# Optimization experiments

Measured on AMD Instinct MI355X. Metric: run time of the kernel, lower is better.

## Reference

```python
import jax, jax.numpy as jnp
import numpy as np

N = 4096          # num_nodes
F = 64            # node_features
H = 128           # hidden_dim
NH = 4            # num_heads
HD = H // NH      # per-head dim = 32
L = 3             # num_layers
C = 7             # num_classes
EDGE_P = 0.004    # ~16 avg degree


def setup_inputs() -> dict:
    key = jax.random.key(0)
    ks = jax.random.split(key, 20)
    g = lambda k, shape, fan_in: jax.random.normal(k, shape, jnp.float32) / np.sqrt(fan_in)
    x = jax.random.normal(ks[0], (N, F), jnp.float32)
    adj = (jax.random.uniform(ks[1], (N, N)) < EDGE_P).astype(jnp.float32)
    return {
        "x": x,
        "adj": adj,
        "enc_W": g(ks[2], (F, H), F), "enc_b": jnp.zeros((H,), jnp.float32),
        "gcn_W": g(ks[3], (L, H, H), H), "gcn_b": jnp.zeros((L, H), jnp.float32),
        "attn_W": g(ks[4], (L, NH, H, HD), H), "attn_Wb": jnp.zeros((L, NH, HD), jnp.float32),
        "attn_a": g(ks[5], (L, NH, 2 * HD), 2 * HD), "attn_ab": jnp.zeros((L, NH), jnp.float32),
        "cls_W1": g(ks[6], (H, H // 2), H), "cls_b1": jnp.zeros((H // 2,), jnp.float32),
        "cls_W2": g(ks[7], (H // 2, C), H // 2), "cls_b2": jnp.zeros((C,), jnp.float32),
        "con_W1": g(ks[8], (H, H // 2), H), "con_b1": jnp.zeros((H // 2,), jnp.float32),
        "con_W2": g(ks[9], (H // 2, 1), H // 2), "con_b2": jnp.zeros((1,), jnp.float32),
    }


def _normalize_adj(adj):
    a = adj + jnp.eye(adj.shape[0], dtype=adj.dtype)
    dinv = jnp.sum(a, axis=1) ** -0.5
    return dinv[:, None] * a * dinv[None, :]


def _gcn(h, adj_norm, W, b):
    support = adj_norm @ h                      # [N,H]
    return jax.nn.relu(support @ W + b)         # dropout=0 (eval)


def _attention(h, edge_mask, W, Wb, a, ab):
    # h:[N,H], W:[NH,H,HD], a:[NH,2*HD]; per-pair score = Linear(concat(h_i,h_j))
    hh = jnp.einsum('nf,hfd->hnd', h, W) + Wb[:, None, :]     # [NH,N,HD]
    a_src, a_dst = a[:, :HD], a[:, HD:]
    s_src = jnp.einsum('hnd,hd->hn', hh, a_src)               # [NH,N]
    s_dst = jnp.einsum('hnd,hd->hn', hh, a_dst)               # [NH,N]
    scores = s_src[:, :, None] + s_dst[:, None, :] + ab[:, None, None]
    # original uses literal 0.0 (NOT -inf) for non-edges before softmax
    scores = jnp.where(edge_mask[None, :, :], scores, 0.0)    # [NH,N,N]
    probs = jax.nn.softmax(scores, axis=-1)
    out = jnp.einsum('hij,hjd->hid', probs, hh)               # [NH,N,HD]
    return out.transpose(1, 0, 2).reshape(h.shape[0], NH * HD)


def reference(x, adj, enc_W, enc_b, gcn_W, gcn_b, attn_W, attn_Wb, attn_a, attn_ab,
              cls_W1, cls_b1, cls_W2, cls_b2, con_W1, con_b1, con_W2, con_b2):
    h = jax.nn.relu(x @ enc_W + enc_b)          # node encoder (dropout=0)
    adj_norm = _normalize_adj(adj)
    edge_mask = adj > 0
    for i in range(L):
        h_gcn = _gcn(h, adj_norm, gcn_W[i], gcn_b[i])
        h_attn = _attention(h, edge_mask, attn_W[i], attn_Wb[i], attn_a[i], attn_ab[i])
        h = jax.nn.relu(h_gcn + h_attn)
    node_logits = jax.nn.relu(h @ cls_W1 + cls_b1) @ cls_W2 + cls_b2
    h_mean = jnp.mean(h, axis=0, keepdims=True)
    contagion = jax.nn.relu(h_mean @ con_W1 + con_b1) @ con_W2 + con_b2
    return (node_logits, h, contagion)
```

## Files before the change

kernel.cpp:

```cpp
#include <hip/hip_runtime.h>

typedef unsigned short u16;
typedef unsigned int u32;

#define N 4096
#define F 64
#define H 128
#define NH 4
#define HD 32
#define EMAX 64

__device__ float g_hA[N * H];
__device__ float g_hB[N * H];
__device__ float g_hhA[N * H];
__device__ float g_hhB[N * H];
__device__ u16   g_cols[N * EMAX];
__device__ int   g_deg[N];
__device__ float g_dinv[N];
__device__ float g_ssrcA[N * NH];
__device__ float g_ssrcB[N * NH];
__device__ float g_sdstA[N * NH];
__device__ float g_sdstB[N * NH];
__device__ float g_part[4][32][H];

__device__ __forceinline__ void agg4(int i0, int tid, const float* __restrict__ h,
                                     const float* __restrict__ hhin,
                                     const float* __restrict__ ssrc_in,
                                     const float* __restrict__ sdst_in,
                                     int l, const float* __restrict__ abv,
                                     int (&jl)[4][EMAX], float (&dv)[4][EMAX],
                                     float (&sdl)[4][EMAX * NH], float (&wl)[4][EMAX * NH],
                                     float (&eml)[4][NH], float (&basel)[4][NH],
                                     float (&Svl)[4][NH],
                                     float& outa0, float& outa1,
                                     float& sup0, float& sup1) {
  int c = tid & 127, rg = tid >> 7, hc = c >> 5;
#pragma unroll
  for (int r = 0; r < 4; ++r) {
    int dd = g_deg[i0 + r];
    const u16* cl = g_cols + (size_t)(i0 + r) * EMAX;
    for (int e = tid; e < dd; e += 256) {
      int j = cl[e];
      jl[r][e] = j;
      dv[r][e] = g_dinv[j];
    }
  }
  __syncthreads();

  {
    int g = tid >> 4, lg = tid & 15, ra = g >> 2, ha = g & 3;
    int dda = g_deg[i0 + ra];
    float M = -INFINITY;
    for (int e = lg; e < dda; e += 16) {
      float s = sdst_in[jl[ra][e] * NH + ha];
      sdl[ra][e * NH + ha] = s;
      M = fmaxf(M, s);
    }
#pragma unroll
    for (int m = 8; m >= 1; m >>= 1) M = fmaxf(M, __shfl_xor(M, m, 64));
    if (lg == 0) {
      float ssrc = ssrc_in[(i0 + ra) * NH + ha];
      float ab = abv[ha];
      float mv = fmaxf(0.f, ssrc + ab + M);
      eml[ra][ha] = expf(-mv);
      basel[ra][ha] = ssrc + ab - mv;
    }
  }
  __syncthreads();

  {
    int g = tid >> 4, lg = tid & 15, ra = g >> 2, ha = g & 3;
    int dda = g_deg[i0 + ra];
    float base = basel[ra][ha];
    float Sp = 0.f;
    for (int e = lg; e < dda; e += 16) {
      float w = expf(base + sdl[ra][e * NH + ha]);
      wl[ra][e * NH + ha] = w;
      Sp += w;
    }
#pragma unroll
    for (int m = 8; m >= 1; m >>= 1) Sp += __shfl_xor(Sp, m, 64);
    if (lg == 0) Svl[ra][ha] = Sp;
  }
  __syncthreads();

  float sumc = 0.f;
  const float* part = &g_part[l][0][0];
#pragma unroll
  for (int s = 0; s < 32; ++s) sumc += part[s * H + c];

  float oa[2], sp[2];
#pragma unroll
  for (int rr = 0; rr < 2; ++rr) {
    int r = rg * 2 + rr;
    int i = i0 + r;
    int dd = g_deg[i];
    float em = eml[r][hc], S = Svl[r][hc];
    float aA = 0.f, aT = 0.f, aG = 0.f;
    int e = 0;
    for (; e + 4 <= dd; e += 4) {
      int j0 = jl[r][e], j1 = jl[r][e + 1], j2 = jl[r][e + 2], j3 = jl[r][e + 3];
      float w0 = wl[r][e * NH + hc],       w1 = wl[r][(e + 1) * NH + hc];
      float w2 = wl[r][(e + 2) * NH + hc], w3 = wl[r][(e + 3) * NH + hc];
      float q0 = hhin[j0 * H + c], q1 = hhin[j1 * H + c];
      float q2 = hhin[j2 * H + c], q3 = hhin[j3 * H + c];
      float p0 = h[j0 * H + c], p1 = h[j1 * H + c];
      float p2 = h[j2 * H + c], p3 = h[j3 * H + c];
      aA = fmaf(w0, q0, aA); aA = fmaf(w1, q1, aA);
      aA = fmaf(w2, q2, aA); aA = fmaf(w3, q3, aA);
      aT += (q0 + q1) + (q2 + q3);
      aG = fmaf(dv[r][e], p0, aG);     aG = fmaf(dv[r][e + 1], p1, aG);
      aG = fmaf(dv[r][e + 2], p2, aG); aG = fmaf(dv[r][e + 3], p3, aG);
    }
    for (; e < dd; ++e) {
      int j = jl[r][e];
      float w = wl[r][e * NH + hc];
      float q = hhin[j * H + c];
      aA = fmaf(w, q, aA);
      aT += q;
      aG = fmaf(dv[r][e], h[j * H + c], aG);
    }
    float Z = S + em * (float)(N - dd);
    oa[rr] = (aA + em * (sumc - aT)) / Z;
    float di = g_dinv[i];
    sp[rr] = di * (aG + di * h[i * H + c]);
  }
  outa0 = oa[0]; outa1 = oa[1]; sup0 = sp[0]; sup1 = sp[1];
}

__device__ __forceinline__ void proj4(int i0, int tid, const float (&hrowT)[H][4],
                                      const float* __restrict__ aW,
                                      const float* __restrict__ aWb,
                                      const float* __restrict__ aa, int lp,
                                      float* __restrict__ hhout,
                                      float* __restrict__ ssrc_out,
                                      float* __restrict__ sdst_out) {
  int c = tid & 127, rg = tid >> 7, hc = c >> 5, dc = c & 31;
  float b = aWb[hc * HD + dc];
  float p0 = b, p1 = b;
  for (int f = 0; f < H; ++f) {
    float w = aW[(hc * H + f) * HD + dc];
    float2 hv = *reinterpret_cast<const float2*>(&hrowT[f][rg * 2]);
    p0 = fmaf(hv.x, w, p0);
    p1 = fmaf(hv.y, w, p1);
  }
  int r0 = i0 + rg * 2, r1 = r0 + 1;
  hhout[r0 * H + c] = p0;
  hhout[r1 * H + c] = p1;
  const float* ap = aa + hc * 2 * HD;
  float as = ap[dc], ad = ap[HD + dc];
  float ss0 = p0 * as, ss1 = p1 * as, sd0 = p0 * ad, sd1 = p1 * ad;
#pragma unroll
  for (int m = 16; m >= 1; m >>= 1) {
    ss0 += __shfl_xor(ss0, m, 64); ss1 += __shfl_xor(ss1, m, 64);
    sd0 += __shfl_xor(sd0, m, 64); sd1 += __shfl_xor(sd1, m, 64);
  }
  if (dc == 0) {
    ssrc_out[r0 * NH + hc] = ss0; ssrc_out[r1 * NH + hc] = ss1;
    sdst_out[r0 * NH + hc] = sd0; sdst_out[r1 * NH + hc] = sd1;
  }
  atomicAdd(&g_part[lp][r0 & 31][c], p0);
  atomicAdd(&g_part[lp][r1 & 31][c], p1);
}

__global__ void k_csr_enc(const float* __restrict__ adj, const float* __restrict__ x,
                          const float* __restrict__ eW, const float* __restrict__ eb,
                          const float* __restrict__ aW, const float* __restrict__ aWb,
                          const float* __restrict__ aa) {
  __shared__ float xT[F][4];
  __shared__ float hrowT[H][4];
  __shared__ int cnt;
  int tid = threadIdx.x;
  if (blockIdx.x < N) {
    int row = blockIdx.x;
    if (tid == 0) cnt = 0;
    __syncthreads();
    int base = tid * 16;
    const float4* p = reinterpret_cast<const float4*>(adj + (size_t)row * N + base);
    float4 q0 = p[0], q1 = p[1], q2 = p[2], q3 = p[3];
    float vals[16] = {q0.x, q0.y, q0.z, q0.w, q1.x, q1.y, q1.z, q1.w,
                      q2.x, q2.y, q2.z, q2.w, q3.x, q3.y, q3.z, q3.w};
#pragma unroll
    for (int t = 0; t < 16; ++t)
      if (vals[t] != 0.f) {
        int pos = atomicAdd(&cnt, 1);
        if (pos < EMAX) g_cols[row * EMAX + pos] = (u16)(base + t);
      }
    __syncthreads();
    if (tid == 0) {
      g_deg[row] = cnt < EMAX ? cnt : EMAX;
      g_dinv[row] = 1.0f / sqrtf((float)(cnt + 1));
    }
  } else {
    int i0 = (blockIdx.x - N) * 4;
    int c = tid & 127, rg = tid >> 7;
    {
      int r = tid >> 6, k = tid & 63;
      xT[k][r] = x[(i0 + r) * F + k];
    }
    __syncthreads();
    float b = eb[c];
    float e0 = b, e1 = b;
    for (int k = 0; k < F; ++k) {
      float w = eW[k * H + c];
      float2 xv = *reinterpret_cast<const float2*>(&xT[k][rg * 2]);
      e0 = fmaf(xv.x, w, e0);
      e1 = fmaf(xv.y, w, e1);
    }
    e0 = fmaxf(e0, 0.f); e1 = fmaxf(e1, 0.f);
    int r0 = i0 + rg * 2, r1 = r0 + 1;
    g_hA[r0 * H + c] = e0; g_hA[r1 * H + c] = e1;
    hrowT[c][rg * 2] = e0; hrowT[c][rg * 2 + 1] = e1;
    __syncthreads();
    proj4(i0, tid, hrowT, aW, aWb, aa, 0, g_hhA, g_ssrcA, g_sdstA);
  }
}

__global__ void k_acp(int pp, int l, const float* __restrict__ gW,
                      const float* __restrict__ gb, const float* __restrict__ aW,
                      const float* __restrict__ aWb, const float* __restrict__ aa,
                      const float* __restrict__ abv) {
  const float* h    = pp ? g_hB : g_hA;
  float*       hout = pp ? g_hA : g_hB;
  const float* hhin = pp ? g_hhB : g_hhA;
  float*       hhout= pp ? g_hhA : g_hhB;
  const float* ssin = pp ? g_ssrcB : g_ssrcA;
  float*       ssout= pp ? g_ssrcA : g_ssrcB;
  const float* sdin = pp ? g_sdstB : g_sdstA;
  float*       sdout= pp ? g_sdstA : g_sdstB;
  __shared__ int   jl[4][EMAX];
  __shared__ float dv[4][EMAX];
  __shared__ float sdl[4][EMAX * NH];
  __shared__ float wl[4][EMAX * NH];
  __shared__ float eml[4][NH], basel[4][NH], Svl[4][NH];
  __shared__ float srowT[H][4];
  __shared__ float hrowT[H][4];
  int i0 = blockIdx.x * 4, tid = threadIdx.x;
  int c = tid & 127, rg = tid >> 7;

  float oa0, oa1, sp0, sp1;
  agg4(i0, tid, h, hhin, ssin, sdin, l, abv, jl, dv, sdl, wl, eml, basel, Svl,
       oa0, oa1, sp0, sp1);
  srowT[c][rg * 2] = sp0; srowT[c][rg * 2 + 1] = sp1;
  __syncthreads();

  float b = gb[c];
  float a0 = b, a1 = b;
  for (int f = 0; f < H; ++f) {
    float w = gW[f * H + c];
    float2 sv = *reinterpret_cast<const float2*>(&srowT[f][rg * 2]);
    a0 = fmaf(sv.x, w, a0);
    a1 = fmaf(sv.y, w, a1);
  }
  float g0 = fmaxf(fmaxf(a0, 0.f) + oa0, 0.f);
  float g1 = fmaxf(fmaxf(a1, 0.f) + oa1, 0.f);
  int r0 = i0 + rg * 2, r1 = r0 + 1;
  hout[r0 * H + c] = g0; hout[r1 * H + c] = g1;
  hrowT[c][rg * 2] = g0; hrowT[c][rg * 2 + 1] = g1;
  __syncthreads();

  proj4(i0, tid, hrowT, aW, aWb, aa, l + 1, hhout, ssout, sdout);
}

__global__ void k_acc(const float* __restrict__ abv, const float* __restrict__ gW,
                      const float* __restrict__ gb,
                      const float* __restrict__ W1, const float* __restrict__ b1,
                      const float* __restrict__ W2, const float* __restrict__ b2,
                      float* __restrict__ out, float* __restrict__ outh) {
  __shared__ int   jl[4][EMAX];
  __shared__ float dv[4][EMAX];
  __shared__ float sdl[4][EMAX * NH];
  __shared__ float wl[4][EMAX * NH];
  __shared__ float eml[4][NH], basel[4][NH], Svl[4][NH];
  __shared__ float srowT[H][4];
  __shared__ float hrowT[H][4];
  __shared__ float tl[4][64];
  int i0 = blockIdx.x * 4, tid = threadIdx.x;
  int c = tid & 127, rg = tid >> 7;

  float oa0, oa1, sp0, sp1;
  agg4(i0, tid, g_hA, g_hhA, g_ssrcA, g_sdstA, 2, abv, jl, dv, sdl, wl, eml, basel,
       Svl, oa0, oa1, sp0, sp1);
  srowT[c][rg * 2] = sp0; srowT[c][rg * 2 + 1] = sp1;
  __syncthreads();

  float b = gb[c];
  float a0 = b, a1 = b;
  for (int f = 0; f < H; ++f) {
    float w = gW[f * H + c];
    float2 sv = *reinterpret_cast<const float2*>(&srowT[f][rg * 2]);
    a0 = fmaf(sv.x, w, a0);
    a1 = fmaf(sv.y, w, a1);
  }
  float g0 = fmaxf(fmaxf(a0, 0.f) + oa0, 0.f);
  float g1 = fmaxf(fmaxf(a1, 0.f) + oa1, 0.f);
  int r0 = i0 + rg * 2, r1 = r0 + 1;
  outh[r0 * H + c] = g0; outh[r1 * H + c] = g1;
  hrowT[c][rg * 2] = g0; hrowT[c][rg * 2 + 1] = g1;
  atomicAdd(&g_part[3][r0 & 31][c], g0);
  atomicAdd(&g_part[3][r1 & 31][c], g1);
  __syncthreads();

  int u = tid & 63, rr4 = tid >> 6;
  float a2 = b1[u];
  for (int f = 0; f < H; ++f) a2 = fmaf(hrowT[f][rr4], W1[f * 64 + u], a2);
  tl[rr4][u] = fmaxf(a2, 0.f);
  __syncthreads();
  if (tid < 28) {
    int r = tid / 7, j = tid - r * 7;
    float p = b2[j];
    for (int v = 0; v < 64; ++v) p = fmaf(tl[r][v], W2[v * 7 + j], p);
    out[(i0 + r) * 7 + j] = p;
  }
}

__global__ void k_contagion(const float* __restrict__ W1, const float* __restrict__ b1,
                            const float* __restrict__ W2, const float* __restrict__ b2,
                            float* __restrict__ out) {
  __shared__ float hm[H];
  __shared__ float tl[64];
  int u = threadIdx.x;
#pragma unroll
  for (int q = 0; q < 2; ++q) {
    int col = u + q * 64;
    float s = 0.f;
#pragma unroll
    for (int sl = 0; sl < 32; ++sl) s += g_part[3][sl][col];
    hm[col] = s * (1.0f / 4096.0f);
  }
  __syncthreads();
  float acc = b1[u];
  for (int f = 0; f < H; ++f) acc = fmaf(hm[f], W1[f * 64 + u], acc);
  tl[u] = fmaxf(acc, 0.f);
  __syncthreads();
  if (u == 0) {
    float p = b2[0];
    for (int v = 0; v < 64; ++v) p = fmaf(tl[v], W2[v], p);
    out[0] = p;
  }
}

extern "C" void kernel_launch(void* const* d_in, const int* in_sizes, int n_in,
                              void* d_out, int out_size, void* d_ws, size_t ws_size,
                              hipStream_t stream) {
  const float* x       = (const float*)d_in[0];
  const float* adj     = (const float*)d_in[1];
  const float* enc_W   = (const float*)d_in[2];
  const float* enc_b   = (const float*)d_in[3];
  const float* gcn_W   = (const float*)d_in[4];
  const float* gcn_b   = (const float*)d_in[5];
  const float* attn_W  = (const float*)d_in[6];
  const float* attn_Wb = (const float*)d_in[7];
  const float* attn_a  = (const float*)d_in[8];
  const float* attn_ab = (const float*)d_in[9];
  const float* cls_W1  = (const float*)d_in[10];
  const float* cls_b1  = (const float*)d_in[11];
  const float* cls_W2  = (const float*)d_in[12];
  const float* cls_b2  = (const float*)d_in[13];
  const float* con_W1  = (const float*)d_in[14];
  const float* con_b1  = (const float*)d_in[15];
  const float* con_W2  = (const float*)d_in[16];
  const float* con_b2  = (const float*)d_in[17];
  (void)in_sizes; (void)n_in; (void)d_ws; (void)ws_size; (void)out_size;

  float* out = (float*)d_out;
  float* outh = out + (size_t)N * 7;
  float* outc = out + (size_t)N * 7 + (size_t)N * H;

  void* zr = nullptr;
  hipGetSymbolAddress(&zr, HIP_SYMBOL(g_part));
  hipMemsetAsync(zr, 0, sizeof(float) * 4 * 32 * H, stream);

  k_csr_enc<<<N + N / 4, 256, 0, stream>>>(adj, x, enc_W, enc_b,
                                           attn_W, attn_Wb, attn_a);
  k_acp<<<N / 4, 256, 0, stream>>>(0, 0, gcn_W, gcn_b,
                                   attn_W + (size_t)1 * NH * H * HD,
                                   attn_Wb + (size_t)1 * NH * HD,
                                   attn_a + (size_t)1 * NH * 2 * HD, attn_ab);
  k_acp<<<N / 4, 256, 0, stream>>>(1, 1, gcn_W + (size_t)1 * H * H, gcn_b + H,
                                   attn_W + (size_t)2 * NH * H * HD,
                                   attn_Wb + (size_t)2 * NH * HD,
                                   attn_a + (size_t)2 * NH * 2 * HD, attn_ab + NH);
  k_acc<<<N / 4, 256, 0, stream>>>(attn_ab + 2 * NH, gcn_W + (size_t)2 * H * H,
                                   gcn_b + 2 * H, cls_W1, cls_b1, cls_W2, cls_b2,
                                   out, outh);
  k_contagion<<<1, 64, 0, stream>>>(con_W1, con_b1, con_W2, con_b2, outc);
}
```

Before: 219.1 us.

## Repack weights into float4-interleaved layout and vectorize per-block GEMV loops

Adds extra blocks to the first kernel that repack the GCN, attention-projection and classifier weights into a layout where each thread reads four consecutive input features as one float4. The shared-memory activation tiles become row-major so activations can also be read as float4. This is meant to cut the number of global and LDS load instructions in the per-block small matmuls. In exchange it adds a repack pass each call and extra global buffers.

```diff
diff --git a/kernel.cpp b/kernel.cpp
--- a/kernel.cpp
+++ b/kernel.cpp
@@ -22,6 +22,9 @@
 __device__ float g_sdstA[N * NH];
 __device__ float g_sdstB[N * NH];
 __device__ float g_part[4][32][H];
+__device__ float g_gWQ[3 * H * H];
+__device__ float g_aWQ[3 * NH * H * HD];
+__device__ float g_W1Q[H * 64];
 
 __device__ __forceinline__ void agg4(int i0, int tid, const float* __restrict__ h,
                                      const float* __restrict__ hhin,
@@ -166,7 +169,8 @@
 __global__ void k_csr_enc(const float* __restrict__ adj, const float* __restrict__ x,
                           const float* __restrict__ eW, const float* __restrict__ eb,
                           const float* __restrict__ aW, const float* __restrict__ aWb,
-                          const float* __restrict__ aa) {
+                          const float* __restrict__ aa, const float* __restrict__ gW,
+                          const float* __restrict__ W1) {
   __shared__ float xT[F][4];
   __shared__ float hrowT[H][4];
   __shared__ int cnt;
@@ -191,7 +195,7 @@
       g_deg[row] = cnt < EMAX ? cnt : EMAX;
       g_dinv[row] = 1.0f / sqrtf((float)(cnt + 1));
     }
-  } else {
+  } else if (blockIdx.x < N + N / 4) {
     int i0 = (blockIdx.x - N) * 4;
     int c = tid & 127, rg = tid >> 7;
     {
@@ -213,11 +217,69 @@
     hrowT[c][rg * 2] = e0; hrowT[c][rg * 2 + 1] = e1;
     __syncthreads();
     proj4(i0, tid, hrowT, aW, aWb, aa, 0, g_hhA, g_ssrcA, g_sdstA);
-  }
-}
-
-__global__ void k_acp(int pp, int l, const float* __restrict__ gW,
-                      const float* __restrict__ gb, const float* __restrict__ aW,
+  } else {
+    int gid = (blockIdx.x - (N + N / 4)) * 256 + tid;
+    if (gid < 3 * H * H) {
+      int l = gid / (H * H), rem = gid % (H * H);
+      int fq = rem >> 9, c = (rem >> 2) & 127, ft = rem & 3;
+      g_gWQ[gid] = gW[(size_t)l * H * H + (4 * fq + ft) * H + c];
+      int hc = c >> 5, dc = c & 31;
+      g_aWQ[gid] = aW[(((size_t)l * NH + hc) * H + (4 * fq + ft)) * HD + dc];
+      if (gid < H * 64) {
+        int fq2 = gid >> 8, u = (gid >> 2) & 63, ft2 = gid & 3;
+        g_W1Q[gid] = W1[(4 * fq2 + ft2) * 64 + u];
+      }
+    }
+  }
+}
+
+__device__ __forceinline__ void gemm2q(const float* __restrict__ s0,
+                                       const float* __restrict__ s1,
+                                       const float4* __restrict__ wq,
+                                       float& a0, float& a1) {
+#pragma unroll 4
+  for (int fq = 0; fq < 32; ++fq) {
+    float4 w  = wq[fq * 128];
+    float4 v0 = *reinterpret_cast<const float4*>(s0 + fq * 4);
+    float4 v1 = *reinterpret_cast<const float4*>(s1 + fq * 4);
+    a0 = fmaf(v0.x, w.x, a0); a0 = fmaf(v0.y, w.y, a0);
+    a0 = fmaf(v0.z, w.z, a0); a0 = fmaf(v0.w, w.w, a0);
+    a1 = fmaf(v1.x, w.x, a1); a1 = fmaf(v1.y, w.y, a1);
+    a1 = fmaf(v1.z, w.z, a1); a1 = fmaf(v1.w, w.w, a1);
+  }
+}
+
+__device__ __forceinline__ void proj4q(int i0, int tid, const float (&hT)[4][H],
+                                       const float4* __restrict__ aq,
+                                       const float* __restrict__ aWb,
+                                       const float* __restrict__ aa, int lp,
+                                       float* __restrict__ hhout,
+                                       float* __restrict__ ssrc_out,
+                                       float* __restrict__ sdst_out) {
+  int c = tid & 127, rg = tid >> 7, hc = c >> 5, dc = c & 31;
+  float b = aWb[hc * HD + dc];
+  float p0 = b, p1 = b;
+  gemm2q(hT[rg * 2], hT[rg * 2 + 1], aq, p0, p1);
+  int r0 = i0 + rg * 2, r1 = r0 + 1;
+  hhout[r0 * H + c] = p0;
+  hhout[r1 * H + c] = p1;
+  const float* ap = aa + hc * 2 * HD;
+  float as = ap[dc], ad = ap[HD + dc];
+  float ss0 = p0 * as, ss1 = p1 * as, sd0 = p0 * ad, sd1 = p1 * ad;
+#pragma unroll
+  for (int m = 16; m >= 1; m >>= 1) {
+    ss0 += __shfl_xor(ss0, m, 64); ss1 += __shfl_xor(ss1, m, 64);
+    sd0 += __shfl_xor(sd0, m, 64); sd1 += __shfl_xor(sd1, m, 64);
+  }
+  if (dc == 0) {
+    ssrc_out[r0 * NH + hc] = ss0; ssrc_out[r1 * NH + hc] = ss1;
+    sdst_out[r0 * NH + hc] = sd0; sdst_out[r1 * NH + hc] = sd1;
+  }
+  atomicAdd(&g_part[lp][r0 & 31][c], p0);
+  atomicAdd(&g_part[lp][r1 & 31][c], p1);
+}
+
+__global__ void k_acp(int pp, int l, const float* __restrict__ gb,
                       const float* __restrict__ aWb, const float* __restrict__ aa,
                       const float* __restrict__ abv) {
   const float* h    = pp ? g_hB : g_hA;
@@ -233,38 +295,34 @@
   __shared__ float sdl[4][EMAX * NH];
   __shared__ float wl[4][EMAX * NH];
   __shared__ float eml[4][NH], basel[4][NH], Svl[4][NH];
-  __shared__ float srowT[H][4];
-  __shared__ float hrowT[H][4];
+  __shared__ float sT[4][H];
+  __shared__ float hT[4][H];
   int i0 = blockIdx.x * 4, tid = threadIdx.x;
   int c = tid & 127, rg = tid >> 7;
 
   float oa0, oa1, sp0, sp1;
   agg4(i0, tid, h, hhin, ssin, sdin, l, abv, jl, dv, sdl, wl, eml, basel, Svl,
        oa0, oa1, sp0, sp1);
-  srowT[c][rg * 2] = sp0; srowT[c][rg * 2 + 1] = sp1;
+  sT[rg * 2][c] = sp0; sT[rg * 2 + 1][c] = sp1;
   __syncthreads();
 
   float b = gb[c];
   float a0 = b, a1 = b;
-  for (int f = 0; f < H; ++f) {
-    float w = gW[f * H + c];
-    float2 sv = *reinterpret_cast<const float2*>(&srowT[f][rg * 2]);
-    a0 = fmaf(sv.x, w, a0);
-    a1 = fmaf(sv.y, w, a1);
-  }
+  const float4* gq = reinterpret_cast<const float4*>(g_gWQ) + (size_t)l * 4096 + c;
+  gemm2q(sT[rg * 2], sT[rg * 2 + 1], gq, a0, a1);
   float g0 = fmaxf(fmaxf(a0, 0.f) + oa0, 0.f);
   float g1 = fmaxf(fmaxf(a1, 0.f) + oa1, 0.f);
   int r0 = i0 + rg * 2, r1 = r0 + 1;
   hout[r0 * H + c] = g0; hout[r1 * H + c] = g1;
-  hrowT[c][rg * 2] = g0; hrowT[c][rg * 2 + 1] = g1;
-  __syncthreads();
-
-  proj4(i0, tid, hrowT, aW, aWb, aa, l + 1, hhout, ssout, sdout);
-}
-
-__global__ void k_acc(const float* __restrict__ abv, const float* __restrict__ gW,
-                      const float* __restrict__ gb,
-                      const float* __restrict__ W1, const float* __restrict__ b1,
+  hT[rg * 2][c] = g0; hT[rg * 2 + 1][c] = g1;
+  __syncthreads();
+
+  const float4* aq = reinterpret_cast<const float4*>(g_aWQ) + (size_t)(l + 1) * 4096 + c;
+  proj4q(i0, tid, hT, aq, aWb, aa, l + 1, hhout, ssout, sdout);
+}
+
+__global__ void k_acc(const float* __restrict__ abv, const float* __restrict__ gb,
+                      const float* __restrict__ b1,
                       const float* __restrict__ W2, const float* __restrict__ b2,
                       float* __restrict__ out, float* __restrict__ outh) {
   __shared__ int   jl[4][EMAX];
@@ -272,8 +330,8 @@
   __shared__ float sdl[4][EMAX * NH];
   __shared__ float wl[4][EMAX * NH];
   __shared__ float eml[4][NH], basel[4][NH], Svl[4][NH];
-  __shared__ float srowT[H][4];
-  __shared__ float hrowT[H][4];
+  __shared__ float sT[4][H];
+  __shared__ float hT[4][H];
   __shared__ float tl[4][64];
   int i0 = blockIdx.x * 4, tid = threadIdx.x;
   int c = tid & 127, rg = tid >> 7;
@@ -281,29 +339,35 @@
   float oa0, oa1, sp0, sp1;
   agg4(i0, tid, g_hA, g_hhA, g_ssrcA, g_sdstA, 2, abv, jl, dv, sdl, wl, eml, basel,
        Svl, oa0, oa1, sp0, sp1);
-  srowT[c][rg * 2] = sp0; srowT[c][rg * 2 + 1] = sp1;
+  sT[rg * 2][c] = sp0; sT[rg * 2 + 1][c] = sp1;
   __syncthreads();
 
   float b = gb[c];
   float a0 = b, a1 = b;
-  for (int f = 0; f < H; ++f) {
-    float w = gW[f * H + c];
-    float2 sv = *reinterpret_cast<const float2*>(&srowT[f][rg * 2]);
-    a0 = fmaf(sv.x, w, a0);
-    a1 = fmaf(sv.y, w, a1);
-  }
+  const float4* gq = reinterpret_cast<const float4*>(g_gWQ) + (size_t)2 * 4096 + c;
+  gemm2q(sT[rg * 2], sT[rg * 2 + 1], gq, a0, a1);
   float g0 = fmaxf(fmaxf(a0, 0.f) + oa0, 0.f);
   float g1 = fmaxf(fmaxf(a1, 0.f) + oa1, 0.f);
   int r0 = i0 + rg * 2, r1 = r0 + 1;
   outh[r0 * H + c] = g0; outh[r1 * H + c] = g1;
-  hrowT[c][rg * 2] = g0; hrowT[c][rg * 2 + 1] = g1;
+  hT[rg * 2][c] = g0; hT[rg * 2 + 1][c] = g1;
   atomicAdd(&g_part[3][r0 & 31][c], g0);
   atomicAdd(&g_part[3][r1 & 31][c], g1);
   __syncthreads();
 
   int u = tid & 63, rr4 = tid >> 6;
   float a2 = b1[u];
-  for (int f = 0; f < H; ++f) a2 = fmaf(hrowT[f][rr4], W1[f * 64 + u], a2);
+  {
+    const float4* w1q = reinterpret_cast<const float4*>(g_W1Q) + u;
+    const float* hr = hT[rr4];
+#pragma unroll 4
+    for (int fq = 0; fq < 32; ++fq) {
+      float4 w  = w1q[fq * 64];
+      float4 hv = *reinterpret_cast<const float4*>(hr + fq * 4);
+      a2 = fmaf(hv.x, w.x, a2); a2 = fmaf(hv.y, w.y, a2);
+      a2 = fmaf(hv.z, w.z, a2); a2 = fmaf(hv.w, w.w, a2);
+    }
+  }
   tl[rr4][u] = fmaxf(a2, 0.f);
   __syncthreads();
   if (tid < 28) {
@@ -371,18 +435,16 @@
   hipGetSymbolAddress(&zr, HIP_SYMBOL(g_part));
   hipMemsetAsync(zr, 0, sizeof(float) * 4 * 32 * H, stream);
 
-  k_csr_enc<<<N + N / 4, 256, 0, stream>>>(adj, x, enc_W, enc_b,
-                                           attn_W, attn_Wb, attn_a);
-  k_acp<<<N / 4, 256, 0, stream>>>(0, 0, gcn_W, gcn_b,
-                                   attn_W + (size_t)1 * NH * H * HD,
+  k_csr_enc<<<N + N / 4 + 192, 256, 0, stream>>>(adj, x, enc_W, enc_b,
+                                                 attn_W, attn_Wb, attn_a,
+                                                 gcn_W, cls_W1);
+  k_acp<<<N / 4, 256, 0, stream>>>(0, 0, gcn_b,
                                    attn_Wb + (size_t)1 * NH * HD,
                                    attn_a + (size_t)1 * NH * 2 * HD, attn_ab);
-  k_acp<<<N / 4, 256, 0, stream>>>(1, 1, gcn_W + (size_t)1 * H * H, gcn_b + H,
-                                   attn_W + (size_t)2 * NH * H * HD,
+  k_acp<<<N / 4, 256, 0, stream>>>(1, 1, gcn_b + H,
                                    attn_Wb + (size_t)2 * NH * HD,
                                    attn_a + (size_t)2 * NH * 2 * HD, attn_ab + NH);
-  k_acc<<<N / 4, 256, 0, stream>>>(attn_ab + 2 * NH, gcn_W + (size_t)2 * H * H,
-                                   gcn_b + 2 * H, cls_W1, cls_b1, cls_W2, cls_b2,
-                                   out, outh);
+  k_acc<<<N / 4, 256, 0, stream>>>(attn_ab + 2 * NH, gcn_b + 2 * H,
+                                   cls_b1, cls_W2, cls_b2, out, outh);
   k_contagion<<<1, 64, 0, stream>>>(con_W1, con_b1, con_W2, con_b2, outc);
 }
```

Result: no change. 218.9 us (-0.1%).
